# Kernel tuning notes

Measured on AMD Instinct MI355X. Metric: run time of the kernel, lower is better.

## Reference

```python
import jax, jax.numpy as jnp
import numpy as np

N = 2_000_000
CLAMP_THR = 0.9999999


def quat_to_rot(q):
    # q: [N,4] (unnormalized) -> [N,3,3] rotation matrices
    q = q / jnp.linalg.norm(q, axis=-1, keepdims=True)
    w, x, y, z = q[:, 0], q[:, 1], q[:, 2], q[:, 3]
    R = jnp.stack([
        jnp.stack([1 - 2 * (y * y + z * z), 2 * (x * y - w * z), 2 * (x * z + w * y)], axis=-1),
        jnp.stack([2 * (x * y + w * z), 1 - 2 * (x * x + z * z), 2 * (y * z - w * x)], axis=-1),
        jnp.stack([2 * (x * z - w * y), 2 * (y * z + w * x), 1 - 2 * (x * x + y * y)], axis=-1),
    ], axis=-2)
    return R


def setup_inputs() -> dict:
    key = jax.random.key(0)
    k1, k2, k3 = jax.random.split(key, 3)
    R_w2c1 = quat_to_rot(jax.random.normal(k1, (N, 4), dtype=jnp.float32))
    R_w2c2 = quat_to_rot(jax.random.normal(k2, (N, 4), dtype=jnp.float32))
    # small-angle noise rotation so residuals are realistic (cos inside clamp)
    q_noise = jnp.concatenate(
        [jnp.ones((N, 1), dtype=jnp.float32), 0.05 * jax.random.normal(k3, (N, 3), dtype=jnp.float32)],
        axis=-1)
    Rn = quat_to_rot(q_noise)
    # R_rel ~= R_w2c2 @ R_w2c1^T composed with noise
    R_rel = jnp.einsum('nij,njk->nik', jnp.einsum('nij,nkj->nik', R_w2c2, R_w2c1), Rn)
    return {"R_rel": R_rel, "R_w2c1": R_w2c1, "R_w2c2": R_w2c2}


def reference(R_rel, R_w2c1, R_w2c2):
    # residual M = R_rel^T @ R_w2c2 @ R_w2c1^T should be identity;
    # cos(theta) = (tr(M) - 1) / 2
    tr = jnp.einsum('nji,njk,nik->n', R_rel, R_w2c2, R_w2c1)
    cos = 0.5 * (tr - 1.0)
    cos_c = jnp.clip(cos, -CLAMP_THR, CLAMP_THR)
    loss = jnp.sum(jnp.arccos(cos_c))[None]  # shape (1,), matching the CUDA buffer
    # analytic gradient of sum arccos(cos) wrt R_w2c1, R_w2c2;
    # zero where the clamp is active (derivative of clip is 0 there)
    g = jnp.where(jnp.abs(cos) < CLAMP_THR,
                  -0.5 / jnp.sqrt(1.0 - cos_c * cos_c),
                  jnp.zeros_like(cos))  # includes d cos / d tr = 0.5
    # d tr / d R_w2c1 = R_rel^T @ R_w2c2 ; d tr / d R_w2c2 = R_rel @ R_w2c1
    d_R_w2c1 = g[:, None, None] * jnp.einsum('nji,njk->nik', R_rel, R_w2c2)
    d_R_w2c2 = g[:, None, None] * jnp.einsum('nij,njk->nik', R_rel, R_w2c1)
    return loss, d_R_w2c1, d_R_w2c2
```

## Files before the change

### kernel.cpp

```cpp
#include <hip/hip_runtime.h>

#define CLAMP_THR 0.9999999f

constexpr int ELEMS = 256;
constexpr int FLTS  = ELEMS * 9;

__global__ void zero_loss_kernel(float* out) {
    if (threadIdx.x == 0) out[0] = 0.0f;
}

__global__ __launch_bounds__(256) void geodesic_grad_kernel(
    const float* __restrict__ Rrel,
    const float* __restrict__ Rw1,
    const float* __restrict__ Rw2,
    float* __restrict__ out,
    int n)
{
    __shared__ float lA[FLTS];
    __shared__ float lB[FLTS];
    __shared__ float lC[FLTS];
    __shared__ float wsum[4];

    const int t = threadIdx.x;
    float* __restrict__ out1 = out + 1;
    float* __restrict__ out2 = out + 1 + (size_t)n * 9;

    float local_loss = 0.0f;
    const int nChunks = (n + ELEMS - 1) / ELEMS;

    for (int c = blockIdx.x; c < nChunks; c += gridDim.x) {
        const size_t base = (size_t)c * FLTS;
        const int valid = min(ELEMS, n - c * ELEMS);
        const int vf = valid * 9;

        if (valid == ELEMS) {
            const float4* gA = reinterpret_cast<const float4*>(Rrel + base);
            const float4* gB = reinterpret_cast<const float4*>(Rw2 + base);
            const float4* gC = reinterpret_cast<const float4*>(Rw1 + base);
            float4* sA = reinterpret_cast<float4*>(lA);
            float4* sB = reinterpret_cast<float4*>(lB);
            float4* sC = reinterpret_cast<float4*>(lC);
            #pragma unroll
            for (int i = t; i < FLTS / 4; i += 256) {
                sA[i] = gA[i];
                sB[i] = gB[i];
                sC[i] = gC[i];
            }
        } else {
            for (int i = t; i < vf; i += 256) {
                lA[i] = Rrel[base + i];
                lB[i] = Rw2[base + i];
                lC[i] = Rw1[base + i];
            }
        }
        __syncthreads();

        if (t < valid) {
            float R[9], A[9], B[9];
            #pragma unroll
            for (int j = 0; j < 9; ++j) {
                R[j] = lA[9 * t + j];
                A[j] = lB[9 * t + j];
                B[j] = lC[9 * t + j];
            }
            float M[9];
            #pragma unroll
            for (int i = 0; i < 3; ++i)
                #pragma unroll
                for (int k = 0; k < 3; ++k)
                    M[3 * i + k] = R[i]     * A[k]
                                 + R[3 + i] * A[3 + k]
                                 + R[6 + i] * A[6 + k];
            float tr = 0.0f;
            #pragma unroll
            for (int j = 0; j < 9; ++j) tr += M[j] * B[j];

            float cosv  = 0.5f * (tr - 1.0f);
            float cosc  = fminf(fmaxf(cosv, -CLAMP_THR), CLAMP_THR);
            local_loss += acosf(cosc);
            float g = (fabsf(cosv) < CLAMP_THR)
                        ? (-0.5f / sqrtf(1.0f - cosc * cosc))
                        : 0.0f;

            #pragma unroll
            for (int j = 0; j < 9; ++j) lA[9 * t + j] = g * M[j];
            #pragma unroll
            for (int i = 0; i < 3; ++i)
                #pragma unroll
                for (int k = 0; k < 3; ++k)
                    lB[9 * t + 3 * i + k] = g * (R[3 * i]     * B[k]
                                               + R[3 * i + 1] * B[3 + k]
                                               + R[3 * i + 2] * B[6 + k]);
        }
        __syncthreads();

        for (int i = t; i < vf; i += 256) {
            out1[base + i] = lA[i];
            out2[base + i] = lB[i];
        }
        __syncthreads();
    }

    #pragma unroll
    for (int off = 32; off > 0; off >>= 1)
        local_loss += __shfl_down(local_loss, off, 64);
    if ((t & 63) == 0) wsum[t >> 6] = local_loss;
    __syncthreads();
    if (t == 0)
        atomicAdd(out, wsum[0] + wsum[1] + wsum[2] + wsum[3]);
}

extern "C" void kernel_launch(void* const* d_in, const int* in_sizes, int n_in,
                              void* d_out, int out_size, void* d_ws, size_t ws_size,
                              hipStream_t stream) {
    const float* Rrel = (const float*)d_in[0];
    const float* Rw1  = (const float*)d_in[1];
    const float* Rw2  = (const float*)d_in[2];
    float* out = (float*)d_out;
    const int n = in_sizes[0] / 9;

    zero_loss_kernel<<<1, 64, 0, stream>>>(out);

    const int nChunks = (n + ELEMS - 1) / ELEMS;
    const int grid = nChunks < 2048 ? nChunks : 2048;
    geodesic_grad_kernel<<<grid, 256, 0, stream>>>(Rrel, Rw1, Rw2, out, n);
}
```

Measured before the change: 301.6 us.

## Launch one block per chunk and vectorize output stores with nontemporal writes

Replaces the grid-stride loop (grid capped at 2048) with one block per 256-element chunk, so each block loads, computes and stores a single tile. Full-chunk outputs, which sit one float off 16-byte alignment because of the loss slot, are now written as aligned 4-wide nontemporal vector stores with scalar head and tail fixups instead of scalar stores. This targets store throughput and streaming cache pollution on a bandwidth-bound kernel. It adds one atomicAdd per block, roughly 7800 in total, and more block launch overhead.

```diff
diff --git a/kernel.cpp b/kernel.cpp
--- a/kernel.cpp
+++ b/kernel.cpp
@@ -2,11 +2,34 @@
 
 #define CLAMP_THR 0.9999999f
 
+typedef float f4 __attribute__((ext_vector_type(4)));
+
 constexpr int ELEMS = 256;
 constexpr int FLTS  = ELEMS * 9;
+constexpr int VEC   = FLTS / 4;
 
 __global__ void zero_loss_kernel(float* out) {
     if (threadIdx.x == 0) out[0] = 0.0f;
+}
+
+__device__ inline void store_chunk(float* __restrict__ dst,
+                                   const float* __restrict__ src, int t)
+{
+    const int i0 = (int)(((16u - ((uintptr_t)dst & 15u)) & 15u) >> 2);
+    const int nv = (FLTS - i0) / 4;
+    f4* __restrict__ v = (f4*)(dst + i0);
+    for (int i = t; i < nv; i += 256) {
+        const int s = 4 * i + i0;
+        f4 x = { src[s], src[s + 1], src[s + 2], src[s + 3] };
+        __builtin_nontemporal_store(x, v + i);
+    }
+    if (t < i0) dst[t] = src[t];
+    const int tb = i0 + 4 * nv;
+    const int ntail = FLTS - tb;
+    if (t >= 4 && t < 4 + ntail) {
+        const int i = tb + (t - 4);
+        dst[i] = src[i];
+    }
 }
 
 __global__ __launch_bounds__(256) void geodesic_grad_kernel(
@@ -22,83 +45,84 @@
     __shared__ float wsum[4];
 
     const int t = threadIdx.x;
+    const int c = blockIdx.x;
+    const size_t base = (size_t)c * FLTS;
+    const int valid = min(ELEMS, n - c * ELEMS);
+    const int vf = valid * 9;
+
     float* __restrict__ out1 = out + 1;
     float* __restrict__ out2 = out + 1 + (size_t)n * 9;
 
+    if (valid == ELEMS) {
+        const f4* __restrict__ gA = (const f4*)(Rrel + base);
+        const f4* __restrict__ gB = (const f4*)(Rw2 + base);
+        const f4* __restrict__ gC = (const f4*)(Rw1 + base);
+        f4* __restrict__ sA = (f4*)lA;
+        f4* __restrict__ sB = (f4*)lB;
+        f4* __restrict__ sC = (f4*)lC;
+        #pragma unroll
+        for (int i = t; i < VEC; i += 256) {
+            sA[i] = gA[i];
+            sB[i] = gB[i];
+            sC[i] = gC[i];
+        }
+    } else {
+        for (int i = t; i < vf; i += 256) {
+            lA[i] = Rrel[base + i];
+            lB[i] = Rw2[base + i];
+            lC[i] = Rw1[base + i];
+        }
+    }
+    __syncthreads();
+
     float local_loss = 0.0f;
-    const int nChunks = (n + ELEMS - 1) / ELEMS;
+    if (t < valid) {
+        float R[9], A[9], B[9];
+        #pragma unroll
+        for (int j = 0; j < 9; ++j) {
+            R[j] = lA[9 * t + j];
+            A[j] = lB[9 * t + j];
+            B[j] = lC[9 * t + j];
+        }
+        float M[9];
+        #pragma unroll
+        for (int i = 0; i < 3; ++i)
+            #pragma unroll
+            for (int k = 0; k < 3; ++k)
+                M[3 * i + k] = R[i]     * A[k]
+                             + R[3 + i] * A[3 + k]
+                             + R[6 + i] * A[6 + k];
+        float tr = 0.0f;
+        #pragma unroll
+        for (int j = 0; j < 9; ++j) tr += M[j] * B[j];
 
-    for (int c = blockIdx.x; c < nChunks; c += gridDim.x) {
-        const size_t base = (size_t)c * FLTS;
-        const int valid = min(ELEMS, n - c * ELEMS);
-        const int vf = valid * 9;
+        float cosv = 0.5f * (tr - 1.0f);
+        float cosc = fminf(fmaxf(cosv, -CLAMP_THR), CLAMP_THR);
+        local_loss = acosf(cosc);
+        float g = (fabsf(cosv) < CLAMP_THR)
+                    ? (-0.5f / sqrtf(1.0f - cosc * cosc))
+                    : 0.0f;
 
-        if (valid == ELEMS) {
-            const float4* gA = reinterpret_cast<const float4*>(Rrel + base);
-            const float4* gB = reinterpret_cast<const float4*>(Rw2 + base);
-            const float4* gC = reinterpret_cast<const float4*>(Rw1 + base);
-            float4* sA = reinterpret_cast<float4*>(lA);
-            float4* sB = reinterpret_cast<float4*>(lB);
-            float4* sC = reinterpret_cast<float4*>(lC);
+        #pragma unroll
+        for (int j = 0; j < 9; ++j) lA[9 * t + j] = g * M[j];
+        #pragma unroll
+        for (int i = 0; i < 3; ++i)
             #pragma unroll
-            for (int i = t; i < FLTS / 4; i += 256) {
-                sA[i] = gA[i];
-                sB[i] = gB[i];
-                sC[i] = gC[i];
-            }
-        } else {
-            for (int i = t; i < vf; i += 256) {
-                lA[i] = Rrel[base + i];
-                lB[i] = Rw2[base + i];
-                lC[i] = Rw1[base + i];
-            }
-        }
-        __syncthreads();
+            for (int k = 0; k < 3; ++k)
+                lB[9 * t + 3 * i + k] = g * (R[3 * i]     * B[k]
+                                           + R[3 * i + 1] * B[3 + k]
+                                           + R[3 * i + 2] * B[6 + k]);
+    }
+    __syncthreads();
 
-        if (t < valid) {
-            float R[9], A[9], B[9];
-            #pragma unroll
-            for (int j = 0; j < 9; ++j) {
-                R[j] = lA[9 * t + j];
-                A[j] = lB[9 * t + j];
-                B[j] = lC[9 * t + j];
-            }
-            float M[9];
-            #pragma unroll
-            for (int i = 0; i < 3; ++i)
-                #pragma unroll
-                for (int k = 0; k < 3; ++k)
-                    M[3 * i + k] = R[i]     * A[k]
-                                 + R[3 + i] * A[3 + k]
-                                 + R[6 + i] * A[6 + k];
-            float tr = 0.0f;
-            #pragma unroll
-            for (int j = 0; j < 9; ++j) tr += M[j] * B[j];
-
-            float cosv  = 0.5f * (tr - 1.0f);
-            float cosc  = fminf(fmaxf(cosv, -CLAMP_THR), CLAMP_THR);
-            local_loss += acosf(cosc);
-            float g = (fabsf(cosv) < CLAMP_THR)
-                        ? (-0.5f / sqrtf(1.0f - cosc * cosc))
-                        : 0.0f;
-
-            #pragma unroll
-            for (int j = 0; j < 9; ++j) lA[9 * t + j] = g * M[j];
-            #pragma unroll
-            for (int i = 0; i < 3; ++i)
-                #pragma unroll
-                for (int k = 0; k < 3; ++k)
-                    lB[9 * t + 3 * i + k] = g * (R[3 * i]     * B[k]
-                                               + R[3 * i + 1] * B[3 + k]
-                                               + R[3 * i + 2] * B[6 + k]);
-        }
-        __syncthreads();
-
+    if (valid == ELEMS) {
+        store_chunk(out1 + base, lA, t);
+        store_chunk(out2 + base, lB, t);
+    } else {
         for (int i = t; i < vf; i += 256) {
             out1[base + i] = lA[i];
             out2[base + i] = lB[i];
         }
-        __syncthreads();
     }
 
     #pragma unroll
@@ -122,6 +146,5 @@
     zero_loss_kernel<<<1, 64, 0, stream>>>(out);
 
     const int nChunks = (n + ELEMS - 1) / ELEMS;
-    const int grid = nChunks < 2048 ? nChunks : 2048;
-    geodesic_grad_kernel<<<grid, 256, 0, stream>>>(Rrel, Rw1, Rw2, out, n);
+    geodesic_grad_kernel<<<nChunks, 256, 0, stream>>>(Rrel, Rw1, Rw2, out, n);
 }
```

Result: slower. 321.2 us (+6.5%).

## Replace LDS-staged grid-stride loop with direct per-thread vector loads and stores

Applied to the files above, without the earlier changes.

Drops the shared-memory staging of 256 matrices per block and the grid-stride loop. Each thread now reads its own three 3x3 matrices straight from global memory with unaligned 4-wide vector loads, and writes both gradients directly. One block is launched per 256 elements. The loss is reduced by writing per-block partial sums to the workspace and summing them in a single-block kernel, which replaces the atomics and the separate zero kernel. This removes LDS traffic and barriers, but per-thread 36-byte strided accesses are less coalesced than the staged float4 copies.

```diff
diff --git a/kernel.cpp b/kernel.cpp
--- a/kernel.cpp
+++ b/kernel.cpp
@@ -2,103 +2,82 @@
 
 #define CLAMP_THR 0.9999999f
 
-constexpr int ELEMS = 256;
-constexpr int FLTS  = ELEMS * 9;
+typedef float f4a __attribute__((ext_vector_type(4), aligned(4)));
 
 __global__ void zero_loss_kernel(float* out) {
     if (threadIdx.x == 0) out[0] = 0.0f;
 }
 
-__global__ __launch_bounds__(256) void geodesic_grad_kernel(
+template<bool USE_WS>
+__global__ __launch_bounds__(256) void geodesic_direct_kernel(
     const float* __restrict__ Rrel,
     const float* __restrict__ Rw1,
     const float* __restrict__ Rw2,
     float* __restrict__ out,
+    float* __restrict__ ws,
     int n)
 {
-    __shared__ float lA[FLTS];
-    __shared__ float lB[FLTS];
-    __shared__ float lC[FLTS];
     __shared__ float wsum[4];
-
     const int t = threadIdx.x;
-    float* __restrict__ out1 = out + 1;
-    float* __restrict__ out2 = out + 1 + (size_t)n * 9;
+    const int e = blockIdx.x * 256 + t;
 
     float local_loss = 0.0f;
-    const int nChunks = (n + ELEMS - 1) / ELEMS;
+    if (e < n) {
+        const size_t b = (size_t)e * 9;
+        float R[9], A[9], B[9];
 
-    for (int c = blockIdx.x; c < nChunks; c += gridDim.x) {
-        const size_t base = (size_t)c * FLTS;
-        const int valid = min(ELEMS, n - c * ELEMS);
-        const int vf = valid * 9;
+        f4a v;
+        v = *(const f4a*)(Rrel + b);     R[0]=v.x; R[1]=v.y; R[2]=v.z; R[3]=v.w;
+        v = *(const f4a*)(Rrel + b + 4); R[4]=v.x; R[5]=v.y; R[6]=v.z; R[7]=v.w;
+        R[8] = Rrel[b + 8];
+        v = *(const f4a*)(Rw2 + b);      A[0]=v.x; A[1]=v.y; A[2]=v.z; A[3]=v.w;
+        v = *(const f4a*)(Rw2 + b + 4);  A[4]=v.x; A[5]=v.y; A[6]=v.z; A[7]=v.w;
+        A[8] = Rw2[b + 8];
+        v = *(const f4a*)(Rw1 + b);      B[0]=v.x; B[1]=v.y; B[2]=v.z; B[3]=v.w;
+        v = *(const f4a*)(Rw1 + b + 4);  B[4]=v.x; B[5]=v.y; B[6]=v.z; B[7]=v.w;
+        B[8] = Rw1[b + 8];
 
-        if (valid == ELEMS) {
-            const float4* gA = reinterpret_cast<const float4*>(Rrel + base);
-            const float4* gB = reinterpret_cast<const float4*>(Rw2 + base);
-            const float4* gC = reinterpret_cast<const float4*>(Rw1 + base);
-            float4* sA = reinterpret_cast<float4*>(lA);
-            float4* sB = reinterpret_cast<float4*>(lB);
-            float4* sC = reinterpret_cast<float4*>(lC);
+        float M[9];
+        #pragma unroll
+        for (int i = 0; i < 3; ++i)
             #pragma unroll
-            for (int i = t; i < FLTS / 4; i += 256) {
-                sA[i] = gA[i];
-                sB[i] = gB[i];
-                sC[i] = gC[i];
-            }
-        } else {
-            for (int i = t; i < vf; i += 256) {
-                lA[i] = Rrel[base + i];
-                lB[i] = Rw2[base + i];
-                lC[i] = Rw1[base + i];
-            }
-        }
-        __syncthreads();
+            for (int k = 0; k < 3; ++k)
+                M[3 * i + k] = R[i]     * A[k]
+                             + R[3 + i] * A[3 + k]
+                             + R[6 + i] * A[6 + k];
+        float tr = 0.0f;
+        #pragma unroll
+        for (int j = 0; j < 9; ++j) tr += M[j] * B[j];
 
-        if (t < valid) {
-            float R[9], A[9], B[9];
+        float cosv = 0.5f * (tr - 1.0f);
+        float cosc = fminf(fmaxf(cosv, -CLAMP_THR), CLAMP_THR);
+        local_loss = acosf(cosc);
+        float g = (fabsf(cosv) < CLAMP_THR)
+                    ? (-0.5f / sqrtf(1.0f - cosc * cosc))
+                    : 0.0f;
+
+        float* __restrict__ o1 = out + 1 + b;
+        f4a s;
+        s.x = g*M[0]; s.y = g*M[1]; s.z = g*M[2]; s.w = g*M[3];
+        *(f4a*)(o1) = s;
+        s.x = g*M[4]; s.y = g*M[5]; s.z = g*M[6]; s.w = g*M[7];
+        *(f4a*)(o1 + 4) = s;
+        o1[8] = g*M[8];
+
+        float D[9];
+        #pragma unroll
+        for (int i = 0; i < 3; ++i)
             #pragma unroll
-            for (int j = 0; j < 9; ++j) {
-                R[j] = lA[9 * t + j];
-                A[j] = lB[9 * t + j];
-                B[j] = lC[9 * t + j];
-            }
-            float M[9];
-            #pragma unroll
-            for (int i = 0; i < 3; ++i)
-                #pragma unroll
-                for (int k = 0; k < 3; ++k)
-                    M[3 * i + k] = R[i]     * A[k]
-                                 + R[3 + i] * A[3 + k]
-                                 + R[6 + i] * A[6 + k];
-            float tr = 0.0f;
-            #pragma unroll
-            for (int j = 0; j < 9; ++j) tr += M[j] * B[j];
-
-            float cosv  = 0.5f * (tr - 1.0f);
-            float cosc  = fminf(fmaxf(cosv, -CLAMP_THR), CLAMP_THR);
-            local_loss += acosf(cosc);
-            float g = (fabsf(cosv) < CLAMP_THR)
-                        ? (-0.5f / sqrtf(1.0f - cosc * cosc))
-                        : 0.0f;
-
-            #pragma unroll
-            for (int j = 0; j < 9; ++j) lA[9 * t + j] = g * M[j];
-            #pragma unroll
-            for (int i = 0; i < 3; ++i)
-                #pragma unroll
-                for (int k = 0; k < 3; ++k)
-                    lB[9 * t + 3 * i + k] = g * (R[3 * i]     * B[k]
-                                               + R[3 * i + 1] * B[3 + k]
-                                               + R[3 * i + 2] * B[6 + k]);
-        }
-        __syncthreads();
-
-        for (int i = t; i < vf; i += 256) {
-            out1[base + i] = lA[i];
-            out2[base + i] = lB[i];
-        }
-        __syncthreads();
+            for (int k = 0; k < 3; ++k)
+                D[3 * i + k] = g * (R[3 * i]     * B[k]
+                                  + R[3 * i + 1] * B[3 + k]
+                                  + R[3 * i + 2] * B[6 + k]);
+        float* __restrict__ o2 = out + 1 + (size_t)n * 9 + b;
+        s.x = D[0]; s.y = D[1]; s.z = D[2]; s.w = D[3];
+        *(f4a*)(o2) = s;
+        s.x = D[4]; s.y = D[5]; s.z = D[6]; s.w = D[7];
+        *(f4a*)(o2 + 4) = s;
+        o2[8] = D[8];
     }
 
     #pragma unroll
@@ -106,8 +85,31 @@
         local_loss += __shfl_down(local_loss, off, 64);
     if ((t & 63) == 0) wsum[t >> 6] = local_loss;
     __syncthreads();
-    if (t == 0)
-        atomicAdd(out, wsum[0] + wsum[1] + wsum[2] + wsum[3]);
+    if (t == 0) {
+        const float blocksum = wsum[0] + wsum[1] + wsum[2] + wsum[3];
+        if (USE_WS) ws[blockIdx.x] = blocksum;
+        else        atomicAdd(out, blocksum);
+    }
+}
+
+__global__ __launch_bounds__(1024) void reduce_loss_kernel(
+    const float* __restrict__ ws, int nb, float* __restrict__ out)
+{
+    __shared__ float wsum[16];
+    const int t = threadIdx.x;
+    float s = 0.0f;
+    for (int i = t; i < nb; i += 1024) s += ws[i];
+    #pragma unroll
+    for (int off = 32; off > 0; off >>= 1)
+        s += __shfl_down(s, off, 64);
+    if ((t & 63) == 0) wsum[t >> 6] = s;
+    __syncthreads();
+    if (t == 0) {
+        float tot = 0.0f;
+        #pragma unroll
+        for (int i = 0; i < 16; ++i) tot += wsum[i];
+        out[0] = tot;
+    }
 }
 
 extern "C" void kernel_launch(void* const* d_in, const int* in_sizes, int n_in,
@@ -118,10 +120,15 @@
     const float* Rw2  = (const float*)d_in[2];
     float* out = (float*)d_out;
     const int n = in_sizes[0] / 9;
+    const int nb = (n + 255) / 256;
 
-    zero_loss_kernel<<<1, 64, 0, stream>>>(out);
-
-    const int nChunks = (n + ELEMS - 1) / ELEMS;
-    const int grid = nChunks < 2048 ? nChunks : 2048;
-    geodesic_grad_kernel<<<grid, 256, 0, stream>>>(Rrel, Rw1, Rw2, out, n);
+    if (ws_size >= (size_t)nb * sizeof(float)) {
+        geodesic_direct_kernel<true><<<nb, 256, 0, stream>>>(
+            Rrel, Rw1, Rw2, out, (float*)d_ws, n);
+        reduce_loss_kernel<<<1, 1024, 0, stream>>>((const float*)d_ws, nb, out);
+    } else {
+        zero_loss_kernel<<<1, 64, 0, stream>>>(out);
+        geodesic_direct_kernel<false><<<nb, 256, 0, stream>>>(
+            Rrel, Rw1, Rw2, out, nullptr, n);
+    }
 }
```

Result: no change. 299.3 us (-0.8%).
